# Kernel optimization log

Measured on AMD Instinct MI355X. Metric: run time of the kernel, lower is better.

Reference implementation:

```python
import jax, jax.numpy as jnp
import numpy as np

LN_EPS = 1e-5

def _normalize(x, axis=-1, eps=1e-12):
    return x / jnp.clip(jnp.linalg.norm(x, axis=axis, keepdims=True), eps)

def setup_inputs() -> dict:
    key = jax.random.key(0)
    ks = jax.random.split(key, 6)
    B, N, D, H = 8192, 50000, 384, 256
    return {
        "embeddings": jax.random.normal(ks[0], (B, D), jnp.float32),
        "s0": jax.random.normal(ks[1], (B, H), jnp.float32),
        "rule_embeddings": jax.random.normal(ks[2], (N, D), jnp.float32),
        "W": jax.random.normal(ks[3], (H, D), jnp.float32) * (1.0 / np.sqrt(D)),
        "b": jax.random.normal(ks[4], (H,), jnp.float32) * 0.02,
        "alpha": jnp.float32(0.1),
        "gamma": jnp.ones((H,), jnp.float32),
        "beta": jnp.zeros((H,), jnp.float32),
        "top_k": 8,
    }

def reference(embeddings, s0, rule_embeddings, W, b, alpha, gamma, beta, top_k):
    # --- RuleLibrary.retrieve ---
    rules_n = _normalize(rule_embeddings)          # library stores normalized embeddings
    q = _normalize(embeddings)                     # [B, D]
    sims = q @ rules_n.T                           # [B, N] cosine similarity
    _, topk_idx = jax.lax.top_k(sims, top_k)       # [B, k]
    topk_sims = jnp.take_along_axis(sims, topk_idx, axis=-1)  # [B, k]
    weights = jax.nn.softmax(topk_sims, axis=-1)   # [B, k]
    gathered = rules_n[topk_idx]                   # [B, k, D]
    rule_context = jnp.einsum("bk,bkd->bd", weights, gathered)  # [B, D]
    # --- RuleInjectionLayer ---
    rule_vec = jax.nn.gelu(rule_context @ W.T + b, approximate=False)  # [B, H]
    x = s0 + alpha * rule_vec
    mu = jnp.mean(x, axis=-1, keepdims=True)
    var = jnp.var(x, axis=-1, keepdims=True)
    s0_aug = (x - mu) * jax.lax.rsqrt(var + LN_EPS) * gamma + beta
    return s0_aug
```

## Files before the change

kernel.cpp:

```cpp
#include <hip/hip_runtime.h>
#include <hip/hip_bf16.h>
#include <stdint.h>

typedef short bf16x8 __attribute__((ext_vector_type(8)));
typedef float f32x4  __attribute__((ext_vector_type(4)));
typedef int   i32x4  __attribute__((ext_vector_type(4)));
typedef int   i32x8  __attribute__((ext_vector_type(8)));

#define D_DIM   384
#define B_ROWS  8192
#define N_RULES 50000
#define NPAD    50176
#define H_DIM   256
#define NRANGE  16
#define RANGE   3136
#define CHUNKS  98
#define SEGCAP  16
#define FLOOR_SIM 0.155f
#define FLOOR_RAW (FLOOR_SIM * 256.0f)

static_assert(NRANGE * RANGE == NPAD, "range split");
static_assert(CHUNKS * 32 == RANGE, "chunk split");

#define OFF_R8    0ll
#define OFF_Q8    (OFF_R8  + (long long)NPAD   * D_DIM)
#define OFF_W     (OFF_Q8  + (long long)B_ROWS * D_DIM)
#define OFF_CNT   (OFF_W   + (long long)H_DIM  * D_DIM * 2)
#define OFF_CAND  (OFF_CNT + (long long)NRANGE * B_ROWS * 4)
#define OFF_RC    (OFF_CAND+ (long long)B_ROWS * NRANGE * SEGCAP * 4)

__device__ __forceinline__ uint16_t f2bf(float f) {
  uint32_t x = __float_as_uint(f);
  return (uint16_t)((x + 0x7FFFu + ((x >> 16) & 1u)) >> 16);
}
__device__ __forceinline__ uint8_t f2fp8(float f) {
  uint32_t b = __float_as_uint(f);
  uint8_t s = (uint8_t)((b >> 24) & 0x80u);
  float a = fabsf(f);
  if (a >= 0.015625f) {
    if (a > 448.f) return s | 0x7E;
    uint32_t x = b & 0x7FFFFFFFu;
    x += 0x7FFFFu + ((x >> 20) & 1u);
    uint32_t e = (x >> 23) - 127u + 7u;
    uint32_t m = (x >> 20) & 7u;
    return s | (uint8_t)((e << 3) | m);
  } else {
    int m = (int)rintf(a * 512.f);
    if (m > 7) return s | 0x08;
    return s | (uint8_t)m;
  }
}
__device__ __forceinline__ void gload_lds16(const void* g, void* s) {
  __builtin_amdgcn_global_load_lds(
      (const __attribute__((address_space(1))) uint32_t*)g,
      (__attribute__((address_space(3))) uint32_t*)s, 16, 0, 0);
}

#define MFMA_SC(a, b, c) \
  __builtin_amdgcn_mfma_scale_f32_16x16x128_f8f6f4( \
      (a), (b), (c), 0, 0, 0, 0x7F7F7F7F, 0, 0x7F7F7F7F)

__global__ __launch_bounds__(256) void k_prep(
    const float* __restrict__ emb, const float* __restrict__ rules,
    const float* __restrict__ W, uint8_t* __restrict__ r8,
    uint8_t* __restrict__ q8, uint16_t* __restrict__ w_bf) {
  const int w = threadIdx.x >> 6, lane = threadIdx.x & 63;
  long long row = (long long)blockIdx.x * 4 + w;
  if (row >= NPAD + B_ROWS) {
    long long r = row - NPAD - B_ROWS;
    const float2* ip = (const float2*)(W + r * D_DIM) + lane * 3;
    uint16_t* op = w_bf + r * D_DIM + lane * 6;
    #pragma unroll
    for (int i = 0; i < 3; ++i) {
      float2 v = ip[i];
      op[2 * i] = f2bf(v.x); op[2 * i + 1] = f2bf(v.y);
    }
    return;
  }
  uint8_t* dst8; const float* src; bool pad = false;
  if (row < NPAD) {
    dst8 = r8 + row * D_DIM; src = rules + row * D_DIM; pad = (row >= N_RULES);
  } else {
    long long rr = row - NPAD;
    dst8 = q8 + rr * D_DIM; src = emb + rr * D_DIM;
  }
  uint16_t* op = (uint16_t*)(dst8 + lane * 6);
  if (pad) { op[0] = 0; op[1] = 0; op[2] = 0; return; }
  const float2* ip = (const float2*)src + lane * 3;
  float v[6]; float ss = 0.f;
  #pragma unroll
  for (int i = 0; i < 3; ++i) {
    float2 t = ip[i];
    v[2 * i] = t.x; v[2 * i + 1] = t.y;
    ss += t.x * t.x + t.y * t.y;
  }
  #pragma unroll
  for (int m = 1; m < 64; m <<= 1) ss += __shfl_xor(ss, m);
  float scale = 16.f / fmaxf(sqrtf(ss), 1e-12f);
  uint8_t b[6];
  #pragma unroll
  for (int i = 0; i < 6; ++i) b[i] = f2fp8(v[i] * scale);
  op[0] = (uint16_t)(b[0] | (b[1] << 8));
  op[1] = (uint16_t)(b[2] | (b[3] << 8));
  op[2] = (uint16_t)(b[4] | (b[5] << 8));
}

__global__ __launch_bounds__(256, 3) void k_simtop(
    const uint8_t* __restrict__ q8, const uint8_t* __restrict__ r8,
    uint32_t* __restrict__ cnt_seg, uint32_t* __restrict__ cand) {
  __shared__ __align__(16) uint8_t Bs[3][32 * D_DIM];
  __shared__ uint32_t Lcnt[256];
  __shared__ uint32_t Lcand[SEGCAP][256];
  const int tid = threadIdx.x;
  const int w = tid >> 6, lane = tid & 63;
  const int n16 = lane & 15, g = lane >> 4;
  const int mt = blockIdx.x, rg = blockIdx.y;
  const int row0 = mt * 256 + w * 64;

  Lcnt[tid] = 0u;

  i32x8 aov[4][3];
  {
    const uint8_t* ab = q8 + (long long)(row0 + n16) * D_DIM + g * 32;
    #pragma unroll
    for (int mi = 0; mi < 4; ++mi)
      #pragma unroll
      for (int j = 0; j < 3; ++j)
        aov[mi][j] = *(const i32x8*)(ab + mi * 16 * D_DIM + j * 128);
  }

  int goff[3], doff[3];
  #pragma unroll
  for (int i = 0; i < 3; ++i) {
    int s = i * 256 + tid;
    int r = s / 24, p = s - r * 24;
    int o = (p & ~7) | ((p & 7) ^ (r & 7));
    goff[i] = r * D_DIM + o * 16;
    doff[i] = s * 16;
  }
  const uint8_t* rbase = r8 + (long long)rg * RANGE * D_DIM;

  int rb[2][2];
  #pragma unroll
  for (int ni = 0; ni < 2; ++ni)
    #pragma unroll
    for (int b = 0; b < 2; ++b) {
      int r = ni * 16 + n16;
      rb[ni][b] = r * D_DIM + (((2 * g + b) ^ (r & 7)) * 16);
    }
  const f32x4 fzero = {0.f, 0.f, 0.f, 0.f};

  #pragma unroll
  for (int i = 0; i < 3; ++i)
    gload_lds16(rbase + goff[i], (char*)&Bs[0][0] + doff[i]);
  #pragma unroll
  for (int i = 0; i < 3; ++i)
    gload_lds16(rbase + (long long)(32 * D_DIM) + goff[i],
                (char*)&Bs[1][0] + doff[i]);

  int cur = 0;
  for (int c = 0; c < CHUNKS; ++c) {
    if (c + 1 < CHUNKS) {
      asm volatile("s_waitcnt vmcnt(3)" ::: "memory");
    } else {
      asm volatile("s_waitcnt vmcnt(0)" ::: "memory");
    }
    __builtin_amdgcn_s_barrier();
    __builtin_amdgcn_sched_barrier(0);

    if (c + 2 < CHUNKS) {
      int nb = cur + 2; if (nb >= 3) nb -= 3;
      const uint8_t* src = rbase + (long long)(c + 2) * (32 * D_DIM);
      char* dst = (char*)&Bs[nb][0];
      #pragma unroll
      for (int i = 0; i < 3; ++i)
        gload_lds16(src + goff[i], dst + doff[i]);
    }
    __builtin_amdgcn_sched_barrier(0);

    const uint8_t* bb = &Bs[cur][0];
    f32x4 acc[4][2];
    #pragma unroll
    for (int mi = 0; mi < 4; ++mi)
      #pragma unroll
      for (int ni = 0; ni < 2; ++ni) acc[mi][ni] = fzero;

    __builtin_amdgcn_s_setprio(1);
    #pragma unroll
    for (int j = 0; j < 3; ++j) {
      i32x4 l0 = *(const i32x4*)(bb + rb[0][0] + j * 128);
      i32x4 h0 = *(const i32x4*)(bb + rb[0][1] + j * 128);
      i32x4 l1 = *(const i32x4*)(bb + rb[1][0] + j * 128);
      i32x4 h1 = *(const i32x4*)(bb + rb[1][1] + j * 128);
      i32x8 b0 = __builtin_shufflevector(l0, h0, 0, 1, 2, 3, 4, 5, 6, 7);
      i32x8 b1 = __builtin_shufflevector(l1, h1, 0, 1, 2, 3, 4, 5, 6, 7);
      #pragma unroll
      for (int mi = 0; mi < 4; ++mi)
        acc[mi][0] = MFMA_SC(aov[mi][j], b0, acc[mi][0]);
      #pragma unroll
      for (int mi = 0; mi < 4; ++mi)
        acc[mi][1] = MFMA_SC(aov[mi][j], b1, acc[mi][1]);
    }
    __builtin_amdgcn_s_setprio(0);

    const int col0 = rg * RANGE + c * 32;
    #pragma unroll
    for (int mi = 0; mi < 4; ++mi)
      #pragma unroll
      for (int ni = 0; ni < 2; ++ni) {
        f32x4 a = acc[mi][ni];
        float mx = fmaxf(fmaxf(a[0], a[1]), fmaxf(a[2], a[3]));
        if (__any(mx > FLOOR_RAW)) {
          #pragma unroll
          for (int r = 0; r < 4; ++r) {
            float v = a[r];
            if (v > FLOOR_RAW) {
              int lr = w * 64 + mi * 16 + g * 4 + r;
              int col = col0 + ni * 16 + n16;
              uint32_t key = ((uint32_t)f2bf(v * (1.f / 256.f)) << 16)
                             | (uint32_t)col;
              uint32_t slot = atomicAdd(&Lcnt[lr], 1u);
              if (slot < SEGCAP) Lcand[slot][lr] = key;
            }
          }
        }
      }

    cur = cur + 1; if (cur >= 3) cur -= 3;
  }

  __syncthreads();
  {
    int n = (int)Lcnt[tid]; if (n > SEGCAP) n = SEGCAP;
    int grow = mt * 256 + tid;
    cnt_seg[rg * B_ROWS + grow] = (uint32_t)n;
    uint32_t* dp = cand + ((long long)grow * (NRANGE * SEGCAP) + rg * SEGCAP);
    #pragma unroll
    for (int i = 0; i < SEGCAP; ++i) dp[i] = Lcand[i][tid];
  }
}

__global__ __launch_bounds__(256) void k_ctx(
    const uint32_t* __restrict__ cnt_seg, const uint32_t* __restrict__ cand,
    const float* __restrict__ rules, uint16_t* __restrict__ rc_bf) {
  const int w = threadIdx.x >> 6, lane = threadIdx.x & 63;
  const long long row = (long long)blockIdx.x * 4 + w;
  uint32_t v[4];
  #pragma unroll
  for (int i = 0; i < 4; ++i) {
    int s = lane + 64 * i;
    int rgi = s >> 4, j = s & 15;
    uint32_t n = cnt_seg[rgi * B_ROWS + (int)row];
    uint32_t cv = cand[row * (NRANGE * SEGCAP) + s];
    v[i] = ((uint32_t)j < n) ? cv : 0u;
  }

  float wv[8]; int wc[8];
  #pragma unroll
  for (int k = 0; k < 8; ++k) {
    uint32_t m01 = (v[0] > v[1]) ? v[0] : v[1];
    uint32_t m23 = (v[2] > v[3]) ? v[2] : v[3];
    uint32_t m = (m01 > m23) ? m01 : m23;
    int ml = lane;
    #pragma unroll
    for (int s = 1; s < 64; s <<= 1) {
      uint32_t om = __shfl_xor(m, s);
      int ol = __shfl_xor(ml, s);
      if (om > m || (om == m && ol < ml)) { m = om; ml = ol; }
    }
    wv[k] = __uint_as_float(m & 0xFFFF0000u);
    wc[k] = (int)(m & 0xFFFFu);
    if (lane == ml) {
      if (v[0] == m) v[0] = 0u;
      else if (v[1] == m) v[1] = 0u;
      else if (v[2] == m) v[2] = 0u;
      else v[3] = 0u;
    }
  }
  float mx = wv[0], ssum = 0.f, wt[8];
  #pragma unroll
  for (int k = 0; k < 8; ++k) { wt[k] = expf(wv[k] - mx); ssum += wt[k]; }
  float inv = 1.f / ssum;

  float rc[6] = {0.f, 0.f, 0.f, 0.f, 0.f, 0.f};
  #pragma unroll
  for (int k = 0; k < 8; ++k) {
    const float2* rp = (const float2*)(rules + (long long)wc[k] * D_DIM) + lane * 3;
    float v6[6]; float ss = 0.f;
    #pragma unroll
    for (int i = 0; i < 3; ++i) {
      float2 t = rp[i];
      v6[2 * i] = t.x; v6[2 * i + 1] = t.y;
      ss += t.x * t.x + t.y * t.y;
    }
    #pragma unroll
    for (int m = 1; m < 64; m <<= 1) ss += __shfl_xor(ss, m);
    float sc = wt[k] * inv / fmaxf(sqrtf(ss), 1e-12f);
    #pragma unroll
    for (int i = 0; i < 6; ++i) rc[i] += sc * v6[i];
  }
  uint16_t* op = rc_bf + row * D_DIM + lane * 6;
  #pragma unroll
  for (int i = 0; i < 6; ++i) op[i] = f2bf(rc[i]);
}

__global__ __launch_bounds__(256, 2) void k_inject(
    const uint16_t* __restrict__ rc_bf, const uint16_t* __restrict__ w_bf,
    const float* __restrict__ s0, const float* __restrict__ bias,
    const float* __restrict__ alpha_p, float* __restrict__ out) {
  __shared__ uint16_t Wls[64 * D_DIM];
  const int tid = threadIdx.x, w = tid >> 6, lane = tid & 63;
  const int n16 = lane & 15, q4 = lane >> 4;
  const int mt = blockIdx.x, nt = blockIdx.y;
  const int row0 = mt * 128 + w * 32;

  bf16x8 afr[2][12];
  {
    const uint16_t* ab = rc_bf + (long long)(row0 + n16) * D_DIM + q4 * 8;
    #pragma unroll
    for (int mi = 0; mi < 2; ++mi)
      #pragma unroll
      for (int ks = 0; ks < 12; ++ks)
        afr[mi][ks] = *(const bf16x8*)(ab + mi * 16 * D_DIM + ks * 32);
  }
  {
    const char* wsrc = (const char*)(w_bf + (long long)nt * 64 * D_DIM);
    #pragma unroll
    for (int i = 0; i < 12; ++i) {
      int s = i * 256 + tid;
      int brow = (s * 87382) >> 22;
      int pos = s - brow * 48;
      int oo = pos - (brow & 7); if (oo < 0) oo += 48;
      gload_lds16(wsrc + brow * 768 + oo * 16, (char*)Wls + s * 16);
    }
  }
  __syncthreads();

  const f32x4 fzero = {0.f, 0.f, 0.f, 0.f};
  f32x4 acc[2][4];
  #pragma unroll
  for (int mi = 0; mi < 2; ++mi)
    #pragma unroll
    for (int ni = 0; ni < 4; ++ni) acc[mi][ni] = fzero;

  const int rot = n16 & 7;
  #pragma unroll
  for (int ks = 0; ks < 12; ++ks) {
    int p = ks * 4 + q4 + rot;
    if (p >= 48) p -= 48;
    #pragma unroll
    for (int ni = 0; ni < 4; ++ni) {
      bf16x8 bfr = *(const bf16x8*)((const char*)Wls + (ni * 16 + n16) * 768 + p * 16);
      acc[0][ni] = __builtin_amdgcn_mfma_f32_16x16x32_bf16(afr[0][ks], bfr, acc[0][ni], 0, 0, 0);
      acc[1][ni] = __builtin_amdgcn_mfma_f32_16x16x32_bf16(afr[1][ks], bfr, acc[1][ni], 0, 0, 0);
    }
  }

  const float alpha = *alpha_p;
  #pragma unroll
  for (int mi = 0; mi < 2; ++mi)
    #pragma unroll
    for (int ni = 0; ni < 4; ++ni)
      #pragma unroll
      for (int r = 0; r < 4; ++r) {
        int row = row0 + mi * 16 + q4 * 4 + r;
        int col = nt * 64 + ni * 16 + n16;
        float pre = acc[mi][ni][r] + bias[col];
        float g = 0.5f * pre * (1.f + erff(pre * 0.70710678118f));
        long long off = (long long)row * H_DIM + col;
        out[off] = s0[off] + alpha * g;
      }
}

__global__ __launch_bounds__(256) void k_ln(
    float* __restrict__ x, const float* __restrict__ gamma,
    const float* __restrict__ beta) {
  const int w = threadIdx.x >> 6, lane = threadIdx.x & 63;
  const long long row = (long long)blockIdx.x * 4 + w;
  float4 v = ((float4*)(x + row * H_DIM))[lane];
  float s = v.x + v.y + v.z + v.w;
  #pragma unroll
  for (int m = 1; m < 64; m <<= 1) s += __shfl_xor(s, m);
  float mu = s * (1.f / 256.f);
  float dx = v.x - mu, dy = v.y - mu, dz = v.z - mu, dw = v.w - mu;
  float ss = dx * dx + dy * dy + dz * dz + dw * dw;
  #pragma unroll
  for (int m = 1; m < 64; m <<= 1) ss += __shfl_xor(ss, m);
  float rs = rsqrtf(ss * (1.f / 256.f) + 1e-5f);
  float4 g = ((const float4*)gamma)[lane];
  float4 b = ((const float4*)beta)[lane];
  v.x = dx * rs * g.x + b.x;
  v.y = dy * rs * g.y + b.y;
  v.z = dz * rs * g.z + b.z;
  v.w = dw * rs * g.w + b.w;
  ((float4*)(x + row * H_DIM))[lane] = v;
}

extern "C" void kernel_launch(void* const* d_in, const int* in_sizes, int n_in,
                              void* d_out, int out_size, void* d_ws, size_t ws_size,
                              hipStream_t stream) {
  const float* emb   = (const float*)d_in[0];
  const float* s0    = (const float*)d_in[1];
  const float* rules = (const float*)d_in[2];
  const float* W     = (const float*)d_in[3];
  const float* bias  = (const float*)d_in[4];
  const float* alpha = (const float*)d_in[5];
  const float* gamma = (const float*)d_in[6];
  const float* beta  = (const float*)d_in[7];
  (void)in_sizes; (void)n_in; (void)out_size; (void)ws_size;

  char* ws = (char*)d_ws;
  uint8_t*  r8   = (uint8_t*)(ws + OFF_R8);
  uint8_t*  q8   = (uint8_t*)(ws + OFF_Q8);
  uint16_t* w_bf = (uint16_t*)(ws + OFF_W);
  uint32_t* cnt_seg = (uint32_t*)(ws + OFF_CNT);
  uint32_t* cand = (uint32_t*)(ws + OFF_CAND);
  uint16_t* rc_bf = (uint16_t*)(ws + OFF_RC);
  float* out = (float*)d_out;

  k_prep<<<14656, 256, 0, stream>>>(emb, rules, W, r8, q8, w_bf);
  k_simtop<<<dim3(32, NRANGE), 256, 0, stream>>>(q8, r8, cnt_seg, cand);
  k_ctx<<<2048, 256, 0, stream>>>(cnt_seg, cand, rules, rc_bf);
  k_inject<<<dim3(64, 4), 256, 0, stream>>>(rc_bf, w_bf, s0, bias, alpha, out);
  k_ln<<<2048, 256, 0, stream>>>(out, gamma, beta);
}
```

Before: 363.9 us.

## Load rule tiles straight from global into registers, dropping the LDS triple buffer

The similarity kernel no longer stages rule chunks in a triple-buffered shared-memory ring with barriers and async global-to-LDS copies. Each wave now reads its B fragments directly from global memory into registers, prefetching the first 16-row half one chunk ahead. The second half is loaded in the same iteration it is consumed. This removes the per-chunk block barriers and the LDS traffic, and the launch-bounds occupancy hint drops from 3 to 2 to leave room for the extra registers. In exchange, all four waves fetch the same chunk redundantly through the caches, occupancy is lower, and load latency on the non-prefetched half is exposed.

```diff
diff --git a/kernel.cpp b/kernel.cpp
--- a/kernel.cpp
+++ b/kernel.cpp
@@ -105,10 +105,9 @@
   op[2] = (uint16_t)(b[4] | (b[5] << 8));
 }
 
-__global__ __launch_bounds__(256, 3) void k_simtop(
+__global__ __launch_bounds__(256, 2) void k_simtop(
     const uint8_t* __restrict__ q8, const uint8_t* __restrict__ r8,
     uint32_t* __restrict__ cnt_seg, uint32_t* __restrict__ cand) {
-  __shared__ __align__(16) uint8_t Bs[3][32 * D_DIM];
   __shared__ uint32_t Lcnt[256];
   __shared__ uint32_t Lcand[SEGCAP][256];
   const int tid = threadIdx.x;
@@ -129,79 +128,47 @@
         aov[mi][j] = *(const i32x8*)(ab + mi * 16 * D_DIM + j * 128);
   }
 
-  int goff[3], doff[3];
-  #pragma unroll
-  for (int i = 0; i < 3; ++i) {
-    int s = i * 256 + tid;
-    int r = s / 24, p = s - r * 24;
-    int o = (p & ~7) | ((p & 7) ^ (r & 7));
-    goff[i] = r * D_DIM + o * 16;
-    doff[i] = s * 16;
-  }
   const uint8_t* rbase = r8 + (long long)rg * RANGE * D_DIM;
-
-  int rb[2][2];
-  #pragma unroll
-  for (int ni = 0; ni < 2; ++ni)
-    #pragma unroll
-    for (int b = 0; b < 2; ++b) {
-      int r = ni * 16 + n16;
-      rb[ni][b] = r * D_DIM + (((2 * g + b) ^ (r & 7)) * 16);
-    }
+  const uint8_t* p0 = rbase + n16 * D_DIM + g * 32;
+  const uint8_t* p1 = rbase + (16 + n16) * D_DIM + g * 32;
   const f32x4 fzero = {0.f, 0.f, 0.f, 0.f};
 
-  #pragma unroll
-  for (int i = 0; i < 3; ++i)
-    gload_lds16(rbase + goff[i], (char*)&Bs[0][0] + doff[i]);
-  #pragma unroll
-  for (int i = 0; i < 3; ++i)
-    gload_lds16(rbase + (long long)(32 * D_DIM) + goff[i],
-                (char*)&Bs[1][0] + doff[i]);
-
-  int cur = 0;
+  i32x8 bnx[3];
+  #pragma unroll
+  for (int j = 0; j < 3; ++j) bnx[j] = *(const i32x8*)(p0 + j * 128);
+
   for (int c = 0; c < CHUNKS; ++c) {
+    const uint8_t* pc1 = p1 + (long long)c * (32 * D_DIM);
+    i32x8 b1[3];
+    #pragma unroll
+    for (int j = 0; j < 3; ++j) b1[j] = *(const i32x8*)(pc1 + j * 128);
+
+    i32x8 b0[3];
+    #pragma unroll
+    for (int j = 0; j < 3; ++j) b0[j] = bnx[j];
+
     if (c + 1 < CHUNKS) {
-      asm volatile("s_waitcnt vmcnt(3)" ::: "memory");
-    } else {
-      asm volatile("s_waitcnt vmcnt(0)" ::: "memory");
-    }
-    __builtin_amdgcn_s_barrier();
-    __builtin_amdgcn_sched_barrier(0);
-
-    if (c + 2 < CHUNKS) {
-      int nb = cur + 2; if (nb >= 3) nb -= 3;
-      const uint8_t* src = rbase + (long long)(c + 2) * (32 * D_DIM);
-      char* dst = (char*)&Bs[nb][0];
-      #pragma unroll
-      for (int i = 0; i < 3; ++i)
-        gload_lds16(src + goff[i], dst + doff[i]);
-    }
-    __builtin_amdgcn_sched_barrier(0);
-
-    const uint8_t* bb = &Bs[cur][0];
+      const uint8_t* pn0 = p0 + (long long)(c + 1) * (32 * D_DIM);
+      #pragma unroll
+      for (int j = 0; j < 3; ++j) bnx[j] = *(const i32x8*)(pn0 + j * 128);
+    }
+
     f32x4 acc[4][2];
     #pragma unroll
     for (int mi = 0; mi < 4; ++mi)
       #pragma unroll
       for (int ni = 0; ni < 2; ++ni) acc[mi][ni] = fzero;
 
-    __builtin_amdgcn_s_setprio(1);
-    #pragma unroll
-    for (int j = 0; j < 3; ++j) {
-      i32x4 l0 = *(const i32x4*)(bb + rb[0][0] + j * 128);
-      i32x4 h0 = *(const i32x4*)(bb + rb[0][1] + j * 128);
-      i32x4 l1 = *(const i32x4*)(bb + rb[1][0] + j * 128);
-      i32x4 h1 = *(const i32x4*)(bb + rb[1][1] + j * 128);
-      i32x8 b0 = __builtin_shufflevector(l0, h0, 0, 1, 2, 3, 4, 5, 6, 7);
-      i32x8 b1 = __builtin_shufflevector(l1, h1, 0, 1, 2, 3, 4, 5, 6, 7);
+    #pragma unroll
+    for (int j = 0; j < 3; ++j)
       #pragma unroll
       for (int mi = 0; mi < 4; ++mi)
-        acc[mi][0] = MFMA_SC(aov[mi][j], b0, acc[mi][0]);
+        acc[mi][0] = MFMA_SC(aov[mi][j], b0[j], acc[mi][0]);
+    #pragma unroll
+    for (int j = 0; j < 3; ++j)
       #pragma unroll
       for (int mi = 0; mi < 4; ++mi)
-        acc[mi][1] = MFMA_SC(aov[mi][j], b1, acc[mi][1]);
-    }
-    __builtin_amdgcn_s_setprio(0);
+        acc[mi][1] = MFMA_SC(aov[mi][j], b1[j], acc[mi][1]);
 
     const int col0 = rg * RANGE + c * 32;
     #pragma unroll
@@ -225,11 +192,8 @@
           }
         }
       }
-
-    cur = cur + 1; if (cur >= 3) cur -= 3;
-  }
-
-  __syncthreads();
+  }
+
   {
     int n = (int)Lcnt[tid]; if (n > SEGCAP) n = SEGCAP;
     int grow = mt * 256 + tid;
```

Measured after the change: 455.6 us. 25.2% more time.

## Split rule ranges finer and switch similarity kernel to double-buffered LDS

Applied to the files above, without the earlier changes.

Doubles the number of rule ranges (NRANGE 16→32, half the chunks per block) so the similarity kernel launches twice as many blocks. It replaces the triple-buffered LDS pipeline with a double buffer that is refilled after a second barrier following the MFMA reads, which cuts LDS use and may allow more resident blocks. The context kernel now merges 512 candidates per row instead of 256. The trade-offs are an extra barrier per chunk, a shallower prefetch, and twice the candidate buffer traffic and top-k merge work.

```diff
diff --git a/kernel.cpp b/kernel.cpp
--- a/kernel.cpp
+++ b/kernel.cpp
@@ -12,10 +12,11 @@
 #define N_RULES 50000
 #define NPAD    50176
 #define H_DIM   256
-#define NRANGE  16
-#define RANGE   3136
-#define CHUNKS  98
+#define NRANGE  32
+#define RANGE   1568
+#define CHUNKS  49
 #define SEGCAP  16
+#define MROWS   256
 #define FLOOR_SIM 0.155f
 #define FLOOR_RAW (FLOOR_SIM * 256.0f)
 
@@ -108,14 +109,14 @@
 __global__ __launch_bounds__(256, 3) void k_simtop(
     const uint8_t* __restrict__ q8, const uint8_t* __restrict__ r8,
     uint32_t* __restrict__ cnt_seg, uint32_t* __restrict__ cand) {
-  __shared__ __align__(16) uint8_t Bs[3][32 * D_DIM];
-  __shared__ uint32_t Lcnt[256];
-  __shared__ uint32_t Lcand[SEGCAP][256];
+  __shared__ __align__(16) uint8_t Bs[2][32 * D_DIM];
+  __shared__ uint32_t Lcnt[MROWS];
+  __shared__ uint32_t Lcand[SEGCAP][MROWS];
   const int tid = threadIdx.x;
   const int w = tid >> 6, lane = tid & 63;
   const int n16 = lane & 15, g = lane >> 4;
   const int mt = blockIdx.x, rg = blockIdx.y;
-  const int row0 = mt * 256 + w * 64;
+  const int row0 = mt * MROWS + w * 64;
 
   Lcnt[tid] = 0u;
 
@@ -158,7 +159,6 @@
     gload_lds16(rbase + (long long)(32 * D_DIM) + goff[i],
                 (char*)&Bs[1][0] + doff[i]);
 
-  int cur = 0;
   for (int c = 0; c < CHUNKS; ++c) {
     if (c + 1 < CHUNKS) {
       asm volatile("s_waitcnt vmcnt(3)" ::: "memory");
@@ -168,26 +168,25 @@
     __builtin_amdgcn_s_barrier();
     __builtin_amdgcn_sched_barrier(0);
 
-    if (c + 2 < CHUNKS) {
-      int nb = cur + 2; if (nb >= 3) nb -= 3;
-      const uint8_t* src = rbase + (long long)(c + 2) * (32 * D_DIM);
-      char* dst = (char*)&Bs[nb][0];
-      #pragma unroll
-      for (int i = 0; i < 3; ++i)
-        gload_lds16(src + goff[i], dst + doff[i]);
-    }
-    __builtin_amdgcn_sched_barrier(0);
-
-    const uint8_t* bb = &Bs[cur][0];
+    const uint8_t* bb = &Bs[c & 1][0];
     f32x4 acc[4][2];
-    #pragma unroll
-    for (int mi = 0; mi < 4; ++mi)
-      #pragma unroll
-      for (int ni = 0; ni < 2; ++ni) acc[mi][ni] = fzero;
-
-    __builtin_amdgcn_s_setprio(1);
-    #pragma unroll
-    for (int j = 0; j < 3; ++j) {
+
+    {
+      i32x4 l0 = *(const i32x4*)(bb + rb[0][0]);
+      i32x4 h0 = *(const i32x4*)(bb + rb[0][1]);
+      i32x4 l1 = *(const i32x4*)(bb + rb[1][0]);
+      i32x4 h1 = *(const i32x4*)(bb + rb[1][1]);
+      i32x8 b0 = __builtin_shufflevector(l0, h0, 0, 1, 2, 3, 4, 5, 6, 7);
+      i32x8 b1 = __builtin_shufflevector(l1, h1, 0, 1, 2, 3, 4, 5, 6, 7);
+      #pragma unroll
+      for (int mi = 0; mi < 4; ++mi)
+        acc[mi][0] = MFMA_SC(aov[mi][0], b0, fzero);
+      #pragma unroll
+      for (int mi = 0; mi < 4; ++mi)
+        acc[mi][1] = MFMA_SC(aov[mi][0], b1, fzero);
+    }
+    #pragma unroll
+    for (int j = 1; j < 3; ++j) {
       i32x4 l0 = *(const i32x4*)(bb + rb[0][0] + j * 128);
       i32x4 h0 = *(const i32x4*)(bb + rb[0][1] + j * 128);
       i32x4 l1 = *(const i32x4*)(bb + rb[1][0] + j * 128);
@@ -201,7 +200,19 @@
       for (int mi = 0; mi < 4; ++mi)
         acc[mi][1] = MFMA_SC(aov[mi][j], b1, acc[mi][1]);
     }
-    __builtin_amdgcn_s_setprio(0);
+
+    asm volatile("s_waitcnt lgkmcnt(0)" ::: "memory");
+    __builtin_amdgcn_s_barrier();
+    __builtin_amdgcn_sched_barrier(0);
+
+    if (c + 2 < CHUNKS) {
+      const uint8_t* src = rbase + (long long)(c + 2) * (32 * D_DIM);
+      char* dst = (char*)&Bs[c & 1][0];
+      #pragma unroll
+      for (int i = 0; i < 3; ++i)
+        gload_lds16(src + goff[i], dst + doff[i]);
+    }
+    __builtin_amdgcn_sched_barrier(0);
 
     const int col0 = rg * RANGE + c * 32;
     #pragma unroll
@@ -225,14 +236,12 @@
           }
         }
       }
-
-    cur = cur + 1; if (cur >= 3) cur -= 3;
   }
 
   __syncthreads();
   {
     int n = (int)Lcnt[tid]; if (n > SEGCAP) n = SEGCAP;
-    int grow = mt * 256 + tid;
+    int grow = mt * MROWS + tid;
     cnt_seg[rg * B_ROWS + grow] = (uint32_t)n;
     uint32_t* dp = cand + ((long long)grow * (NRANGE * SEGCAP) + rg * SEGCAP);
     #pragma unroll
@@ -245,9 +254,9 @@
     const float* __restrict__ rules, uint16_t* __restrict__ rc_bf) {
   const int w = threadIdx.x >> 6, lane = threadIdx.x & 63;
   const long long row = (long long)blockIdx.x * 4 + w;
-  uint32_t v[4];
-  #pragma unroll
-  for (int i = 0; i < 4; ++i) {
+  uint32_t v[8];
+  #pragma unroll
+  for (int i = 0; i < 8; ++i) {
     int s = lane + 64 * i;
     int rgi = s >> 4, j = s & 15;
     uint32_t n = cnt_seg[rgi * B_ROWS + (int)row];
@@ -260,7 +269,11 @@
   for (int k = 0; k < 8; ++k) {
     uint32_t m01 = (v[0] > v[1]) ? v[0] : v[1];
     uint32_t m23 = (v[2] > v[3]) ? v[2] : v[3];
-    uint32_t m = (m01 > m23) ? m01 : m23;
+    uint32_t m45 = (v[4] > v[5]) ? v[4] : v[5];
+    uint32_t m67 = (v[6] > v[7]) ? v[6] : v[7];
+    uint32_t ma = (m01 > m23) ? m01 : m23;
+    uint32_t mb = (m45 > m67) ? m45 : m67;
+    uint32_t m = (ma > mb) ? ma : mb;
     int ml = lane;
     #pragma unroll
     for (int s = 1; s < 64; s <<= 1) {
@@ -274,7 +287,11 @@
       if (v[0] == m) v[0] = 0u;
       else if (v[1] == m) v[1] = 0u;
       else if (v[2] == m) v[2] = 0u;
-      else v[3] = 0u;
+      else if (v[3] == m) v[3] = 0u;
+      else if (v[4] == m) v[4] = 0u;
+      else if (v[5] == m) v[5] = 0u;
+      else if (v[6] == m) v[6] = 0u;
+      else v[7] = 0u;
     }
   }
   float mx = wv[0], ssum = 0.f, wt[8];
```

Measured after the change: 365.9 us. No clear change (+0.6%).
